# Kernel optimization log

Measured on AMD Instinct MI355X. Metric: run time of the kernel, lower is better.

The kernel has to match this reference:

```python
import jax, jax.numpy as jnp
import numpy as np
import math

B, S, D = 4, 2048, 768
H = 12
DH = D // H  # 64


def setup_inputs() -> dict:
    key = jax.random.key(0)
    ks = jax.random.split(key, 10)
    sc = 1.0 / math.sqrt(D)
    x = jax.random.normal(ks[0], (B, S, D), dtype=jnp.float32)
    # per-head QKV weights stacked: [H, D, DH]; biases [H, DH]
    Wq = jax.random.normal(ks[1], (H, D, DH), dtype=jnp.float32) * sc
    bq = jnp.zeros((H, DH), dtype=jnp.float32)
    Wk = jax.random.normal(ks[2], (H, D, DH), dtype=jnp.float32) * sc
    bk = jnp.zeros((H, DH), dtype=jnp.float32)
    Wv = jax.random.normal(ks[3], (H, D, DH), dtype=jnp.float32) * sc
    bv = jnp.zeros((H, DH), dtype=jnp.float32)
    # output projection: maps concat(all_head) [H*DH] -> D
    Wo = jax.random.normal(ks[4], (H * DH, D), dtype=jnp.float32) * sc
    bo = jnp.zeros((D,), dtype=jnp.float32)
    return {"x": x, "Wq": Wq, "bq": bq, "Wk": Wk, "bk": bk,
            "Wv": Wv, "bv": bv, "Wo": Wo, "bo": bo}


def reference(x, Wq, bq, Wk, bk, Wv, bv, Wo, bo):
    # Batched over heads: equivalent to the per-head Python loop in the original.
    q = jnp.einsum('bnd,hde->bhne', x, Wq) + bq[None, :, None, :]
    k = jnp.einsum('bnd,hde->bhne', x, Wk) + bk[None, :, None, :]
    v = jnp.einsum('bnd,hde->bhne', x, Wv) + bv[None, :, None, :]
    scores = jnp.einsum('bhne,bhme->bhnm', q, k) / jnp.sqrt(jnp.asarray(DH, x.dtype))
    probs = jax.nn.softmax(scores, axis=-1)  # [B,H,S,S] dominant intermediate
    ctx = jnp.einsum('bhnm,bhme->bhne', probs, v)  # [B,H,S,DH]
    # concat heads along feature dim -> [B,S,H*DH]
    ctx = jnp.transpose(ctx, (0, 2, 1, 3)).reshape(x.shape[0], x.shape[1], H * DH)
    out = ctx @ Wo + bo
    return out
```

## Files before the change

### kernel.cpp

```cpp
#include <hip/hip_runtime.h>
#include <hip/hip_bf16.h>
#include <stdint.h>

typedef __bf16 bf16;
typedef bf16 bf16x8 __attribute__((ext_vector_type(8)));
typedef bf16 bf16x4 __attribute__((ext_vector_type(4)));
typedef short s16x4 __attribute__((ext_vector_type(4)));
typedef float f32x4 __attribute__((ext_vector_type(4)));

#define B_   4
#define S_   2048
#define D_   768
#define H_   12
#define DH_  64
#define M_   (B_ * S_)

#define QSCALE (0.125f * 1.44269504088896f)
#define SM_SHIFT 12.0f

#define MFMA32(a, b, c) __builtin_amdgcn_mfma_f32_16x16x32_bf16(a, b, c, 0, 0, 0)
#if __has_builtin(__builtin_amdgcn_mfma_f32_16x16x16_bf16)
#define MFMA16(a, b, c) __builtin_amdgcn_mfma_f32_16x16x16_bf16(a, b, c, 0, 0, 0)
#else
#define MFMA16(a, b, c) __builtin_amdgcn_mfma_f32_16x16x16bf16_1k( \
    __builtin_bit_cast(s16x4, a), __builtin_bit_cast(s16x4, b), c, 0, 0, 0)
#endif

#if __has_builtin(__builtin_amdgcn_exp2f)
#define EXP2(x) __builtin_amdgcn_exp2f(x)
#else
#define EXP2(x) exp2f(x)
#endif

__device__ __forceinline__ float scrub(float v) { return (v == v) ? v : 0.0f; }

__device__ __forceinline__ bf16x4 pack4(float p0, float p1, float p2, float p3) {
    union { uint32_t u[2]; bf16x4 v; } o;
    uint32_t a0 = __builtin_bit_cast(uint32_t, p0) + 0x8000u;
    uint32_t a1 = __builtin_bit_cast(uint32_t, p1) + 0x8000u;
    uint32_t a2 = __builtin_bit_cast(uint32_t, p2) + 0x8000u;
    uint32_t a3 = __builtin_bit_cast(uint32_t, p3) + 0x8000u;
    o.u[0] = __builtin_amdgcn_perm(a1, a0, 0x07060302u);
    o.u[1] = __builtin_amdgcn_perm(a3, a2, 0x07060302u);
    return o.v;
}

__device__ __forceinline__ int swz(int row, int col8) {
    return row * 64 + ((col8 ^ (row & 7)) << 3);
}

#if __has_builtin(__builtin_amdgcn_global_load_lds)
#define ASYNC_STAGE 1
#endif
__device__ __forceinline__ void stage16(bf16* ldsbase, const bf16* g) {
#ifdef ASYNC_STAGE
    __builtin_amdgcn_global_load_lds(
        (const __attribute__((address_space(1))) void*)g,
        (__attribute__((address_space(3))) void*)ldsbase, 16, 0, 0);
#else
    int l = threadIdx.x & 63;
    *(uint4*)(ldsbase + l * 8) = *(const uint4*)g;
#endif
}

__global__ void prep(const void* __restrict__ x,
                     const void* __restrict__ Wq, const void* __restrict__ Wk,
                     const void* __restrict__ Wv, const void* __restrict__ Wo,
                     const void* __restrict__ bq, const void* __restrict__ bk,
                     const void* __restrict__ bv, const void* __restrict__ bo,
                     bf16* __restrict__ Xb, bf16* __restrict__ WTc,
                     bf16* __restrict__ WoT, float* __restrict__ biasC,
                     float* __restrict__ boF, int* __restrict__ flg)
{
    __shared__ int cnt[256];
    __shared__ int isb_sh;
    __shared__ float T[64][65];
    const int tid = threadIdx.x;
    {
        const uint32_t* xw = (const uint32_t*)x;
        int c = 0;
        for (int i = tid * 16; i < tid * 16 + 16; i++) {
            uint32_t e = (xw[i] >> 7) & 0xFFu;
            c += (e >= 100u && e <= 150u) ? 1 : 0;
        }
        cnt[tid] = c;
    }
    __syncthreads();
    if (tid == 0) {
        int t = 0;
        for (int i = 0; i < 256; i++) t += cnt[i];
        isb_sh = (t > 2458) ? 1 : 0;
        if (blockIdx.x == 0) flg[0] = isb_sh;
    }
    __syncthreads();
    const int isb = isb_sh;
    const int blk = blockIdx.x;

    if (blk < 3072) {
        int i = (blk * 256 + tid) * 8;
        if (isb) {
            *(uint4*)(Xb + i) = *(const uint4*)((const bf16*)x + i);
        } else {
            const float4* s = (const float4*)((const float*)x + i);
            float4 f0 = s[0], f1 = s[1];
            bf16x8 v;
            v[0] = (bf16)f0.x; v[1] = (bf16)f0.y; v[2] = (bf16)f0.z; v[3] = (bf16)f0.w;
            v[4] = (bf16)f1.x; v[5] = (bf16)f1.y; v[6] = (bf16)f1.z; v[7] = (bf16)f1.w;
            *(bf16x8*)(Xb + i) = v;
        }
    } else if (blk < 3648) {
        int g = blk - 3072;
        int dt = g % 12, hn = (g / 12) % 12, z = g / 144;
        const void* src = (z == 0) ? Wq : (z == 1) ? Wk : (z == 2) ? Wv : Wo;
        {
            int row = tid >> 2, c = (tid & 3) * 16;
            size_t sbase = (z < 3) ? ((size_t)hn * D_ + dt * 64 + row) * 64 + c
                                   : ((size_t)(dt * 64 + row)) * D_ + hn * 64 + c;
            if (isb) { const bf16* s = (const bf16*)src + sbase;
                #pragma unroll
                for (int j = 0; j < 16; j++) T[row][c + j] = (float)s[j];
            } else { const float* s = (const float*)src + sbase;
                #pragma unroll
                for (int j = 0; j < 16; j++) T[row][c + j] = s[j];
            }
        }
        __syncthreads();
        {
            int rr = tid >> 2, cc = (tid & 3) * 16;
            bf16x8 v0, v1;
            #pragma unroll
            for (int j = 0; j < 8; j++) { v0[j] = (bf16)T[cc + j][rr]; v1[j] = (bf16)T[cc + 8 + j][rr]; }
            bf16* dst = (z < 3) ? WTc : WoT;
            size_t dbase = (z < 3) ? ((size_t)(z * D_ + hn * 64 + rr)) * D_ + dt * 64 + cc
                                   : ((size_t)(hn * 64 + rr)) * D_ + dt * 64 + cc;
            *(bf16x8*)(dst + dbase) = v0;
            *(bf16x8*)(dst + dbase + 8) = v1;
        }
    } else {
        int i = (blk - 3648) * 256 + tid;
        if (i < 3072) {
            const void* src; float* dst; int j, di;
            if (i < 2304) { int p = i / 768; j = i - p * 768;
                src = (p == 0) ? bq : (p == 1) ? bk : bv; dst = biasC; di = i; }
            else { src = bo; j = i - 2304; dst = boF; di = j; }
            dst[di] = isb ? (float)((const bf16*)src)[j] : ((const float*)src)[j];
        }
    }
}

template<int MODE>
__global__ __launch_bounds__(256) void gemm128(
    const bf16* __restrict__ A, const bf16* __restrict__ BT,
    const float* __restrict__ bias,
    bf16* __restrict__ Qo, bf16* __restrict__ Ko, bf16* __restrict__ Vt,
    void* __restrict__ out, const int* __restrict__ flagp)
{
    constexpr int BN = (MODE == 0) ? 128 : 64;
    constexpr int NI = (MODE == 0) ? 4 : 2;
    __shared__ bf16 smem[2 * 128 * 64 + 2 * BN * 64];

    const int mt = blockIdx.x, nt = blockIdx.y;
    const int tid = threadIdx.x, lane = tid & 63, w = tid >> 6;
    const int quad = lane >> 4, ln = lane & 15;
    const int wm = w & 1, wn = w >> 1;

    f32x4 acc[4][NI] = {};
    const int rl = lane >> 3;
    const int cb = (lane & 7) ^ rl;

    const bf16* Ap = A  + (size_t)(mt * 128 + rl) * D_ + cb * 8;
    const bf16* Bp = BT + (size_t)(nt * BN + rl) * D_ + cb * 8;

    auto gstage = [&](int buf, const bf16* ap, const bf16* bp) {
        bf16* al = smem + buf * (128 * 64);
        bf16* bl = smem + 2 * 128 * 64 + buf * (BN * 64);
        #pragma unroll
        for (int j = 0; j < 4; j++)
            stage16(al + (w * 32 + j * 8) * 64, ap + (size_t)(w * 32 + j * 8) * D_);
        #pragma unroll
        for (int j = 0; j < BN / 32; j++)
            stage16(bl + (w * (BN / 4) + j * 8) * 64, bp + (size_t)(w * (BN / 4) + j * 8) * D_);
    };

    gstage(0, Ap, Bp);
    int cur = 0;
    for (int ks = 0; ks < D_; ks += 64) {
        __syncthreads();
        Ap += 64; Bp += 64;
        if (ks + 64 < D_) gstage(cur ^ 1, Ap, Bp);
        const bf16* Ac = smem + cur * (128 * 64);
        const bf16* Bc = smem + 2 * 128 * 64 + cur * (BN * 64);
        #pragma unroll
        for (int kc = 0; kc < 2; kc++) {
            bf16x8 a[4], b[NI];
            #pragma unroll
            for (int i = 0; i < 4; i++)
                a[i] = *(const bf16x8*)(Ac + swz(wm * 64 + i * 16 + ln, (kc << 2) | quad));
            #pragma unroll
            for (int i = 0; i < NI; i++)
                b[i] = *(const bf16x8*)(Bc + swz(wn * (BN / 2) + i * 16 + ln, (kc << 2) | quad));
            #pragma unroll
            for (int mi = 0; mi < 4; mi++)
                #pragma unroll
                for (int ni = 0; ni < NI; ni++)
                    acc[mi][ni] = MFMA32(a[mi], b[ni], acc[mi][ni]);
        }
        cur ^= 1;
    }

    if constexpr (MODE == 0) {
        const int nbase = nt * 128 + wn * 64;
        if (nt < 12) {
            const int proj = nbase / 768;
            const int nh = (nbase % 768) >> 6;
            const float scale = (proj == 0) ? QSCALE : 1.0f;
            bf16* dst = (proj == 0) ? Qo : Ko;
            #pragma unroll
            for (int ni = 0; ni < 4; ni++) {
                int e = ni * 16 + ln;
                float bb = bias[nbase + e];
                #pragma unroll
                for (int mi = 0; mi < 4; mi++)
                    #pragma unroll
                    for (int r = 0; r < 4; r++) {
                        int m = mt * 128 + wm * 64 + mi * 16 + quad * 4 + r;
                        int bi = m >> 11, s = m & (S_ - 1);
                        float v = scrub((acc[mi][ni][r] + bb) * scale);
                        dst[((size_t)(bi * H_ + nh) * S_ + s) * 64 + e] = (bf16)v;
                    }
            }
        } else {
            __syncthreads();
            bf16* epi = smem;
            #pragma unroll
            for (int ni = 0; ni < 4; ni++) {
                float bb = bias[nbase + ni * 16 + ln];
                int row = wn * 64 + ni * 16 + ln;
                #pragma unroll
                for (int mi = 0; mi < 4; mi++)
                    #pragma unroll
                    for (int r = 0; r < 4; r++) {
                        int scol = wm * 64 + mi * 16 + quad * 4 + r;
                        epi[row * 136 + scol] = (bf16)scrub(acc[mi][ni][r] + bb);
                    }
            }
            __syncthreads();
            const int bi = (mt * 128) >> 11, s0 = (mt * 128) & (S_ - 1);
            const int nh0 = ((nt * 128) % 768) >> 6;
            #pragma unroll
            for (int pass = 0; pass < 8; pass++) {
                int row2 = pass * 16 + (tid >> 4);
                int sl = (tid & 15) * 8;
                uint4 v = *(const uint4*)(epi + row2 * 136 + sl);
                int head = row2 >> 6, e = row2 & 63;
                *(uint4*)(Vt + ((size_t)(bi * H_ + nh0 + head) * 64 + e) * S_ + s0 + sl) = v;
            }
        }
    } else {
        const int isb = flagp[0];
        #pragma unroll
        for (int ni = 0; ni < NI; ni++) {
            int n = nt * 64 + wn * 32 + ni * 16 + ln;
            float bb = bias[n];
            #pragma unroll
            for (int mi = 0; mi < 4; mi++)
                #pragma unroll
                for (int r = 0; r < 4; r++) {
                    int m = mt * 128 + wm * 64 + mi * 16 + quad * 4 + r;
                    float v = scrub(acc[mi][ni][r] + bb);
                    if (isb) ((bf16*)out)[(size_t)m * D_ + n] = (bf16)v;
                    else     ((float*)out)[(size_t)m * D_ + n] = v;
                }
        }
    }
}

__global__ __launch_bounds__(256)
__attribute__((amdgpu_waves_per_eu(3, 3)))
void attn(
    const bf16* __restrict__ Q, const bf16* __restrict__ K, const bf16* __restrict__ Vt,
    bf16* __restrict__ ctx)
{
    __shared__ bf16 Kl[2][64 * 64];
    __shared__ bf16 Vl[2][64 * 64];

    const int qt = blockIdx.x, bh = blockIdx.y;
    const int tid = threadIdx.x, lane = tid & 63, w = tid >> 6;
    const int quad = lane >> 4, ln = lane & 15;
    const size_t base = (size_t)bh * (S_ * 64);

    bf16x8 qf[2][2];
    #pragma unroll
    for (int s = 0; s < 2; s++) {
        int qrow = qt * 128 + w * 32 + s * 16 + ln;
        qf[s][0] = *(const bf16x8*)(Q + base + (size_t)qrow * 64 + quad * 8);
        qf[s][1] = *(const bf16x8*)(Q + base + (size_t)qrow * 64 + 32 + quad * 8);
    }

    const f32x4 cinit = {-SM_SHIFT, -SM_SHIFT, -SM_SHIFT, -SM_SHIFT};
    bf16x4 vone;
    vone[0] = (bf16)1.0f; vone[1] = (bf16)1.0f; vone[2] = (bf16)1.0f; vone[3] = (bf16)1.0f;

    f32x4 acc[2][4] = {};
    f32x4 accl[2] = {};

    const int rl = lane >> 3, cb = (lane & 7) ^ rl;
    const bf16* Kg = K  + base + (size_t)rl * 64 + cb * 8;
    const bf16* Vg = Vt + base + (size_t)rl * S_ + cb * 8;

    auto stageKV = [&](bf16* kl, bf16* vl, const bf16* kg, const bf16* vg) {
        #pragma unroll
        for (int j = 0; j < 2; j++) {
            int rbase = w * 16 + j * 8;
            stage16(kl + rbase * 64, kg + (size_t)rbase * 64);
            stage16(vl + rbase * 64, vg + (size_t)rbase * S_);
        }
    };
    auto body = [&](const bf16* Kc, const bf16* Vc) {
        #pragma unroll
        for (int nt = 0; nt < 4; nt++) {
            int br = nt * 16 + ln;
            bf16x8 k0 = *(const bf16x8*)(Kc + swz(br, quad));
            bf16x8 k1 = *(const bf16x8*)(Kc + swz(br, 4 | quad));
            bf16x4 vf[4];
            int c8 = (nt << 1) | (quad >> 1);
            #pragma unroll
            for (int et = 0; et < 4; et++) {
                int vr = et * 16 + ln;
                vf[et] = *(const bf16x4*)(Vc + vr * 64 + (((c8 ^ (vr & 7)) << 3) | ((quad & 1) << 2)));
            }
            #pragma unroll
            for (int s = 0; s < 2; s++) {
                f32x4 zz = MFMA32(k0, qf[s][0], cinit);
                zz = MFMA32(k1, qf[s][1], zz);
                bf16x4 pf = pack4(EXP2(zz[0]), EXP2(zz[1]), EXP2(zz[2]), EXP2(zz[3]));
                accl[s] = MFMA16(pf, vone, accl[s]);
                #pragma unroll
                for (int et = 0; et < 4; et++)
                    acc[s][et] = MFMA16(pf, vf[et], acc[s][et]);
            }
        }
    };

    stageKV(Kl[0], Vl[0], Kg, Vg);
    for (int kt = 0; kt < S_; kt += 128) {
        __syncthreads();
        stageKV(Kl[1], Vl[1], Kg + 64 * 64, Vg + 64);
        body(Kl[0], Vl[0]);
        __syncthreads();
        if (kt + 128 < S_) stageKV(Kl[0], Vl[0], Kg + 128 * 64, Vg + 128);
        body(Kl[1], Vl[1]);
        Kg += 128 * 64; Vg += 128;
    }

    const int bb = bh / H_, hh = bh - bb * H_;
    #pragma unroll
    for (int s = 0; s < 2; s++) {
        float linv[4];
        #pragma unroll
        for (int r = 0; r < 4; r++)
            linv[r] = 1.0f / accl[s][r];
        #pragma unroll
        for (int et = 0; et < 4; et++) {
            int e = et * 16 + ln;
            #pragma unroll
            for (int r = 0; r < 4; r++) {
                int srow_o = qt * 128 + w * 32 + s * 16 + quad * 4 + r;
                float v = scrub(acc[s][et][r] * linv[r]);
                ctx[((size_t)(bb * S_ + srow_o) * H_ + hh) * 64 + e] = (bf16)v;
            }
        }
    }
}

extern "C" void kernel_launch(void* const* d_in, const int* in_sizes, int n_in,
                              void* d_out, int out_size, void* d_ws, size_t ws_size,
                              hipStream_t stream) {
    const void* x  = d_in[0];
    const void* Wq = d_in[1];
    const void* bq = d_in[2];
    const void* Wk = d_in[3];
    const void* bk = d_in[4];
    const void* Wv = d_in[5];
    const void* bv = d_in[6];
    const void* Wo = d_in[7];
    const void* bo = d_in[8];

    char* ws = (char*)d_ws;
    bf16* Qb   = (bf16*)(ws);
    bf16* Kb   = (bf16*)(ws + 12582912);
    bf16* Vtb  = (bf16*)(ws + 25165824);
    bf16* Xb   = (bf16*)(ws + 37748736);
    bf16* Cb   = Xb;
    bf16* WTc  = (bf16*)(ws + 50331648);
    bf16* WoT  = (bf16*)(ws + 53870592);
    int*  flg  = (int*) (ws + 55050240);
    float* bC  = (float*)(ws + 55050496);
    float* boF = (float*)(ws + 55059712);
    (void)in_sizes; (void)n_in; (void)out_size; (void)ws_size;

    prep<<<3660, 256, 0, stream>>>(x, Wq, Wk, Wv, Wo, bq, bk, bv, bo,
                                   Xb, WTc, WoT, bC, boF, flg);

    gemm128<0><<<dim3(M_ / 128, 2304 / 128), 256, 0, stream>>>(
        Xb, WTc, bC, Qb, Kb, Vtb, nullptr, flg);

    attn<<<dim3(S_ / 128, B_ * H_), 256, 0, stream>>>(Qb, Kb, Vtb, Cb);

    gemm128<1><<<dim3(M_ / 128, D_ / 64), 256, 0, stream>>>(
        Cb, WoT, boF, nullptr, nullptr, nullptr, d_out, flg);
}
```

Before: 216.3 us.

## Use 16x16x32 MFMA for PV product via permuted K row mapping

Replaces the 16x16x16 MFMAs for the P·V and row-sum products with 16x16x32 MFMAs. It does this by processing two key sub-tiles together and permuting which K rows each lane computes, so that the packed exp values line up with 8-wide V fragments. K is staged with an extra XOR swizzle to match the new row pattern and avoid LDS bank conflicts, and the MFMA block is wrapped in s_setprio. This halves the number of PV MFMA instructions, at the cost of more registers held for K and V fragments.

```diff
diff --git a/kernel.cpp b/kernel.cpp
--- a/kernel.cpp
+++ b/kernel.cpp
@@ -5,7 +5,6 @@
 typedef __bf16 bf16;
 typedef bf16 bf16x8 __attribute__((ext_vector_type(8)));
 typedef bf16 bf16x4 __attribute__((ext_vector_type(4)));
-typedef short s16x4 __attribute__((ext_vector_type(4)));
 typedef float f32x4 __attribute__((ext_vector_type(4)));
 
 #define B_   4
@@ -19,12 +18,6 @@
 #define SM_SHIFT 12.0f
 
 #define MFMA32(a, b, c) __builtin_amdgcn_mfma_f32_16x16x32_bf16(a, b, c, 0, 0, 0)
-#if __has_builtin(__builtin_amdgcn_mfma_f32_16x16x16_bf16)
-#define MFMA16(a, b, c) __builtin_amdgcn_mfma_f32_16x16x16_bf16(a, b, c, 0, 0, 0)
-#else
-#define MFMA16(a, b, c) __builtin_amdgcn_mfma_f32_16x16x16bf16_1k( \
-    __builtin_bit_cast(s16x4, a), __builtin_bit_cast(s16x4, b), c, 0, 0, 0)
-#endif
 
 #if __has_builtin(__builtin_amdgcn_exp2f)
 #define EXP2(x) __builtin_amdgcn_exp2f(x)
@@ -47,6 +40,9 @@
 
 __device__ __forceinline__ int swz(int row, int col8) {
     return row * 64 + ((col8 ^ (row & 7)) << 3);
+}
+__device__ __forceinline__ int swzK(int row, int col8) {
+    return row * 64 + (((col8 ^ (row & 7) ^ (((row >> 3) & 1) << 2))) << 3);
 }
 
 #if __has_builtin(__builtin_amdgcn_global_load_lds)
@@ -298,47 +294,60 @@
     }
 
     const f32x4 cinit = {-SM_SHIFT, -SM_SHIFT, -SM_SHIFT, -SM_SHIFT};
-    bf16x4 vone;
-    vone[0] = (bf16)1.0f; vone[1] = (bf16)1.0f; vone[2] = (bf16)1.0f; vone[3] = (bf16)1.0f;
+    bf16x8 vone8;
+    #pragma unroll
+    for (int i = 0; i < 8; i++) vone8[i] = (bf16)1.0f;
 
     f32x4 acc[2][4] = {};
     f32x4 accl[2] = {};
 
-    const int rl = lane >> 3, cb = (lane & 7) ^ rl;
-    const bf16* Kg = K  + base + (size_t)rl * 64 + cb * 8;
-    const bf16* Vg = Vt + base + (size_t)rl * S_ + cb * 8;
+    const int rl = lane >> 3;
+    const int cbv = (lane & 7) ^ rl;
+    const bf16* Kg = K  + base + (size_t)rl * 64;
+    const bf16* Vg = Vt + base + (size_t)rl * S_ + cbv * 8;
 
     auto stageKV = [&](bf16* kl, bf16* vl, const bf16* kg, const bf16* vg) {
         #pragma unroll
         for (int j = 0; j < 2; j++) {
             int rbase = w * 16 + j * 8;
-            stage16(kl + rbase * 64, kg + (size_t)rbase * 64);
+            int cbk = (lane & 7) ^ rl ^ ((j & 1) << 2);
+            stage16(kl + rbase * 64, kg + (size_t)rbase * 64 + cbk * 8);
             stage16(vl + rbase * 64, vg + (size_t)rbase * S_);
         }
     };
+
     auto body = [&](const bf16* Kc, const bf16* Vc) {
         #pragma unroll
-        for (int nt = 0; nt < 4; nt++) {
-            int br = nt * 16 + ln;
-            bf16x8 k0 = *(const bf16x8*)(Kc + swz(br, quad));
-            bf16x8 k1 = *(const bf16x8*)(Kc + swz(br, 4 | quad));
-            bf16x4 vf[4];
-            int c8 = (nt << 1) | (quad >> 1);
+        for (int p = 0; p < 2; p++) {
+            bf16x8 k[2][2];
+            #pragma unroll
+            for (int t = 0; t < 2; t++) {
+                int br = p * 32 + ((ln >> 2) << 3) + (t << 2) + (ln & 3);
+                k[t][0] = *(const bf16x8*)(Kc + swzK(br, quad));
+                k[t][1] = *(const bf16x8*)(Kc + swzK(br, 4 | quad));
+            }
+            bf16x8 vf[4];
             #pragma unroll
             for (int et = 0; et < 4; et++) {
                 int vr = et * 16 + ln;
-                vf[et] = *(const bf16x4*)(Vc + vr * 64 + (((c8 ^ (vr & 7)) << 3) | ((quad & 1) << 2)));
-            }
+                vf[et] = *(const bf16x8*)(Vc + swz(vr, (p << 2) | quad));
+            }
+            __builtin_amdgcn_s_setprio(1);
             #pragma unroll
             for (int s = 0; s < 2; s++) {
-                f32x4 zz = MFMA32(k0, qf[s][0], cinit);
-                zz = MFMA32(k1, qf[s][1], zz);
-                bf16x4 pf = pack4(EXP2(zz[0]), EXP2(zz[1]), EXP2(zz[2]), EXP2(zz[3]));
-                accl[s] = MFMA16(pf, vone, accl[s]);
+                f32x4 z0 = MFMA32(k[0][0], qf[s][0], cinit);
+                z0 = MFMA32(k[0][1], qf[s][1], z0);
+                f32x4 z1 = MFMA32(k[1][0], qf[s][0], cinit);
+                z1 = MFMA32(k[1][1], qf[s][1], z1);
+                union { bf16x4 h[2]; bf16x8 v; } pf;
+                pf.h[0] = pack4(EXP2(z0[0]), EXP2(z0[1]), EXP2(z0[2]), EXP2(z0[3]));
+                pf.h[1] = pack4(EXP2(z1[0]), EXP2(z1[1]), EXP2(z1[2]), EXP2(z1[3]));
+                accl[s] = MFMA32(pf.v, vone8, accl[s]);
                 #pragma unroll
                 for (int et = 0; et < 4; et++)
-                    acc[s][et] = MFMA16(pf, vf[et], acc[s][et]);
-            }
+                    acc[s][et] = MFMA32(pf.v, vf[et], acc[s][et]);
+            }
+            __builtin_amdgcn_s_setprio(0);
         }
     };
 
```

Result: faster. 207.9 us (-3.9%).
